# Optimization experiments

Hardware: AMD Instinct MI355X
Metric: run time of the kernel (lower is better)

Reference implementation:

```python
import jax, jax.numpy as jnp
import numpy as np

VTH = 1.0
BRANCH = 2
START_TIME = 10
CODING_TIME = 10
REMAIN_TIME = 5
GAMMA = 0.5
LENS = 0.5


@jax.custom_vjp
def spike_fn(x):
    # Heaviside forward, gaussian surrogate gradient (DH-SNN ActFun_adp)
    return (x > 0).astype(x.dtype)


def _spike_fwd(x):
    return spike_fn(x), x


def _spike_bwd(x, g):
    grad = GAMMA * jnp.exp(-x * x / (2.0 * LENS * LENS)) / np.float32(np.sqrt(2 * np.pi) * LENS)
    return (g * grad,)


spike_fn.defvjp(_spike_fwd, _spike_bwd)


def setup_inputs() -> dict:
    B, T, I, H, O = 2048, 1000, 40, 16, 2
    key = jax.random.key(0)
    ks = jax.random.split(key, 6)
    x = jax.random.normal(ks[0], (B, T, I), jnp.float32)
    target = jax.random.randint(ks[1], (B, T), 0, O, jnp.int32)
    # branch connectivity mask: each neuron's inputs randomly permuted, split across branches
    rng = np.random.default_rng(0)
    mask = np.zeros((H * BRANCH, I), np.float32)
    per = I // BRANCH
    for n in range(H):
        perm = rng.permutation(I)
        for b in range(BRANCH):
            mask[n * BRANCH + b, perm[b * per:(b + 1) * per]] = 1.0
    bound1 = 1.0 / np.sqrt(I)
    W1 = jax.random.uniform(ks[2], (H * BRANCH, I), jnp.float32, -bound1, bound1)
    tau_m = jax.random.uniform(ks[3], (H,), jnp.float32, 0.0, 4.0)
    tau_n = jax.random.uniform(ks[4], (H, BRANCH), jnp.float32, 2.0, 6.0)
    w2k, b2k = jax.random.split(ks[5])
    bound2 = 1.0 / np.sqrt(H)
    W2 = jax.random.uniform(w2k, (O, H), jnp.float32, -bound2, bound2)
    b2 = jax.random.uniform(b2k, (O,), jnp.float32, -bound2, bound2)
    return {"x": x, "target": target, "W1": W1, "tau_m": tau_m,
            "tau_n": tau_n, "mask": jnp.asarray(mask), "W2": W2, "b2": b2}


def reference(x, target, W1, tau_m, tau_n, mask, W2, b2):
    B, T, I = x.shape
    H, BR = tau_n.shape
    Wm = W1 * mask                     # [H*BR, I] masked dendritic weights
    alpha = jax.nn.sigmoid(tau_m)      # [H]  membrane decay
    beta = jax.nn.sigmoid(tau_n)       # [H, BR]  dendritic decay
    idx = jnp.arange(T)
    flags = ((idx - START_TIME) % (CODING_TIME + REMAIN_TIME) > REMAIN_TIME) & (idx > START_TIME)

    def step(carry, xs):
        d, mem, spk = carry
        xt, tgt, flag = xs             # xt [B,I], tgt [B], flag scalar bool
        cur = (xt @ Wm.T).reshape(B, H, BR)
        d = beta * d + (1.0 - beta) * cur
        l = d.sum(-1)                  # [B,H]
        mem = (mem - VTH * spk) * alpha + (1.0 - alpha) * l
        spk = spike_fn(mem - VTH)
        logits = spk @ W2.T + b2       # [B,2]
        p = jax.nn.softmax(logits, axis=1)
        # original applies CrossEntropyLoss to an already-softmaxed output (double softmax)
        ce = -jnp.take_along_axis(jax.nn.log_softmax(p, axis=1), tgt[:, None], axis=1).mean()
        corr = (jnp.argmax(p, axis=1) == tgt).sum()
        loss_inc = jnp.where(flag, ce, jnp.float32(0.0))
        corr_inc = jnp.where(flag, corr, 0)
        return (d, mem, spk), (logits, loss_inc, corr_inc)

    d0 = jnp.zeros((B, H, BR), x.dtype)
    m0 = jnp.zeros((B, H), x.dtype)
    s0 = jnp.zeros((B, H), x.dtype)
    _, (logits_t, loss_t, corr_t) = jax.lax.scan(
        step, (d0, m0, s0), (x.transpose(1, 0, 2), target.T, flags))
    loss = loss_t.sum()
    d2_output = logits_t.transpose(1, 0, 2)  # [B, T, 2]
    correct = corr_t.sum()
    total = flags.sum() * B
    return loss, d2_output, correct, total
```

## Files before the change

### kernel.cpp

```cpp
#include <hip/hip_runtime.h>

#define T_STEPS 1000
#define B_TOT   2048
#define I_IN    40
#define H_N     16
#define TC      25
#define NCHUNK  40
#define EPB     2
#define BLOCK   256
#define ELEM_LDS   (TC*48)
#define CHUNK_LDS  (EPB*ELEM_LDS)
#define NUNIT      (EPB*TC*10)
#define LOGITS_OFF 1
#define CORR_OFF  (1 + 2*B_TOT*T_STEPS)
#define TOTAL_OFF (CORR_OFF + 1)

__global__ void snn_init(float* out) {
    out[0] = 0.0f;
    out[CORR_OFF] = 0.0f;
    out[TOTAL_OFF] = 1216512.0f;
}

__device__ __forceinline__ float dpp_xor1(float v) {
    return __int_as_float(__builtin_amdgcn_update_dpp(0, __float_as_int(v), 0xB1, 0xF, 0xF, true));
}
__device__ __forceinline__ float dpp_xor2(float v) {
    return __int_as_float(__builtin_amdgcn_update_dpp(0, __float_as_int(v), 0x4E, 0xF, 0xF, true));
}
__device__ __forceinline__ float swz_xor4(float v) {
    return __int_as_float(__builtin_amdgcn_ds_swizzle(__float_as_int(v), 0x101F));
}

__global__ __launch_bounds__(BLOCK) void snn_main(
    const float* __restrict__ x, const int* __restrict__ target,
    const float* __restrict__ W1, const float* __restrict__ tau_m,
    const float* __restrict__ tau_n, const float* __restrict__ mask,
    const float* __restrict__ W2, const float* __restrict__ b2,
    float* __restrict__ out)
{
    __shared__ float xbuf[2][CHUNK_LDS];
    __shared__ unsigned smask[EPB*2*TC];

    const int tid  = threadIdx.x;
    const int g    = tid >> 7;
    const int lane = tid & 63;
    const int h    = (tid >> 6) & 1;
    const int q    = lane & 3;
    const int br   = (lane >> 2) & 1;
    const int nl   = lane >> 3;
    const int n    = h*8 + nl;
    const int r    = n*2 + br;
    const int b0   = blockIdx.x * EPB;

    float w[10];
#pragma unroll
    for (int j = 0; j < 10; ++j) {
        const int i = 4*j + q;
        w[j] = W1[r*I_IN + i] * mask[r*I_IN + i];
    }

    const float alpha = 1.0f / (1.0f + __expf(-tau_m[n]));
    const float beta  = 1.0f / (1.0f + __expf(-tau_n[r]));
    const float b2v0  = b2[0];
    const float b2v1  = b2[1];

    float w20[H_N], w21[H_N];
#pragma unroll
    for (int nn = 0; nn < H_N; ++nn) {
        w20[nn] = W2[nn];
        w21[nn] = W2[H_N + nn];
    }

    int goff0, lds0, goff1 = 0, lds1 = 0;
    const bool v1ok = (tid + BLOCK) < NUNIT;
    {
        const int u = tid, e = u/250, rem = u%250, tf = rem/10, f4 = rem%10;
        goff0 = ((b0+e)*T_STEPS + tf)*I_IN + 4*f4;
        lds0  = e*ELEM_LDS + tf*48 + f4;
    }
    if (v1ok) {
        const int u = tid + BLOCK, e = u/250, rem = u%250, tf = rem/10, f4 = rem%10;
        goff1 = ((b0+e)*T_STEPS + tf)*I_IN + 4*f4;
        lds1  = e*ELEM_LDS + tf*48 + f4;
    }

    float4 pf0 = *(const float4*)(x + goff0);
    float4 pf1 = v1ok ? *(const float4*)(x + goff1) : make_float4(0,0,0,0);

    const int  p    = tid >> 2;
    const bool comb = ((tid & 3) == 0) && (p < EPB*TC);
    const int  cg   = p / TC, ct = p % TC;

    float d_st = 0.0f, mem = 0.0f, spk = 0.0f;
    float acc_loss = 0.0f, acc_corr = 0.0f;
    unsigned long long cap = 0;

    for (int c = 0; c < NCHUNK; ++c) {
        const int t0 = c * TC;
        float* buf = xbuf[c & 1];
        buf[lds0] = pf0.x; buf[lds0+12] = pf0.y; buf[lds0+24] = pf0.z; buf[lds0+36] = pf0.w;
        if (v1ok) { buf[lds1] = pf1.x; buf[lds1+12] = pf1.y; buf[lds1+24] = pf1.z; buf[lds1+36] = pf1.w; }
        __syncthreads();
        if (c + 1 < NCHUNK) {
            const int tadd = (t0 + TC) * I_IN;
            pf0 = *(const float4*)(x + tadd + goff0);
            if (v1ok) pf1 = *(const float4*)(x + tadd + goff1);
        }

        const float* xg = buf + g*ELEM_LDS + q*12;
#pragma unroll
        for (int tt = 0; tt < TC; ++tt) {
            const float* xp = xg + tt*48;
            const float4 a0 = *(const float4*)(xp);
            const float4 a1 = *(const float4*)(xp + 4);
            const float2 a2 = *(const float2*)(xp + 8);
            float s = 0.0f;
            s = fmaf(w[0], a0.x, s); s = fmaf(w[1], a0.y, s);
            s = fmaf(w[2], a0.z, s); s = fmaf(w[3], a0.w, s);
            s = fmaf(w[4], a1.x, s); s = fmaf(w[5], a1.y, s);
            s = fmaf(w[6], a1.z, s); s = fmaf(w[7], a1.w, s);
            s = fmaf(w[8], a2.x, s); s = fmaf(w[9], a2.y, s);
            const float s01 = s + dpp_xor1(s);
            const float cur = s01 + dpp_xor2(s01);
            d_st = fmaf(beta, d_st - cur, cur);
            const float l = d_st + swz_xor4(d_st);
            mem = fmaf(alpha, (mem - spk) - l, l);
            const bool fired = mem > 1.0f;
            spk = fired ? 1.0f : 0.0f;
            const unsigned long long bal = __ballot(fired);
            if (lane == tt) cap = bal;
        }

        if (lane < TC) {
            unsigned m8 = 0;
#pragma unroll
            for (int k = 0; k < 8; ++k)
                m8 |= ((unsigned)(cap >> (k*8)) & 1u) << k;
            smask[(g*2 + h)*TC + lane] = m8;
        }
        __syncthreads();

        if (comb) {
            const int t = t0 + ct;
            const unsigned m = smask[(cg*2 + 0)*TC + ct] | (smask[(cg*2 + 1)*TC + ct] << 8);
            float sL0 = b2v0, sL1 = b2v1;
#pragma unroll
            for (int nn = 0; nn < H_N; ++nn) {
                const float f = (float)((m >> nn) & 1u);
                sL0 = fmaf(f, w20[nn], sL0);
                sL1 = fmaf(f, w21[nn], sL1);
            }
            const int b = b0 + cg;
            const int oidx = (b*T_STEPS + t)*2;
            out[LOGITS_OFF + oidx]     = sL0;
            out[LOGITS_OFF + oidx + 1] = sL1;
            const bool flag = (t > 10) && (((t - 10) % 15) > 5);
            if (flag) {
                const int tgt = target[b*T_STEPS + t];
                float mx  = fmaxf(sL0, sL1);
                float e0  = __expf(sL0 - mx), e1 = __expf(sL1 - mx);
                float inv = 1.0f / (e0 + e1);
                float p0  = e0*inv, p1 = e1*inv;
                float mm  = fmaxf(p0, p1);
                float lse = mm + __logf(__expf(p0 - mm) + __expf(p1 - mm));
                float qv  = ((tgt == 1) ? p1 : p0) - lse;
                acc_loss -= qv;
                const int pred = (p1 > p0) ? 1 : 0;
                acc_corr += (pred == tgt) ? 1.0f : 0.0f;
            }
        }
    }

    acc_loss *= (1.0f / (float)B_TOT);
#pragma unroll
    for (int mk = 1; mk < 64; mk <<= 1) {
        acc_loss += __shfl_xor(acc_loss, mk, 64);
        acc_corr += __shfl_xor(acc_corr, mk, 64);
    }
    if (lane == 0) {
        atomicAdd(out, acc_loss);
        atomicAdd(out + CORR_OFF, acc_corr);
    }
}

extern "C" void kernel_launch(void* const* d_in, const int* in_sizes, int n_in,
                              void* d_out, int out_size, void* d_ws, size_t ws_size,
                              hipStream_t stream) {
    const float* x      = (const float*)d_in[0];
    const int*   target = (const int*)d_in[1];
    const float* W1     = (const float*)d_in[2];
    const float* tau_m  = (const float*)d_in[3];
    const float* tau_n  = (const float*)d_in[4];
    const float* mask   = (const float*)d_in[5];
    const float* W2     = (const float*)d_in[6];
    const float* b2     = (const float*)d_in[7];
    float* out = (float*)d_out;

    snn_init<<<1, 1, 0, stream>>>(out);
    snn_main<<<B_TOT/EPB, BLOCK, 0, stream>>>(x, target, W1, tau_m, tau_n, mask, W2, b2, out);
}
```

Measured before the change: 560.4 us.

## Map one batch element per wavefront with packed FMA and lane-local spike history

Changes the thread mapping so that each 64-lane wavefront handles one whole batch element (16 neurons × 2 branches × 2 input halves) instead of splitting it across two waves, and puts four elements in each block. The dot product uses packed v_pk_fma_f32 over pairs of inputs. Branch reduction is now DPP add-combines, replacing the ds_swizzle. Spike history is kept as a per-lane bit register read back with readlane, which removes the ballot, the shared spike-mask array and the second __syncthreads per chunk. This cuts cross-wave synchronisation and instruction count per step, at the cost of more LDS per block (fewer resident blocks) and longer per-lane FMA chains.

```diff
diff --git a/kernel.cpp b/kernel.cpp
--- a/kernel.cpp
+++ b/kernel.cpp
@@ -6,7 +6,7 @@
 #define H_N     16
 #define TC      25
 #define NCHUNK  40
-#define EPB     2
+#define EPB     4
 #define BLOCK   256
 #define ELEM_LDS   (TC*48)
 #define CHUNK_LDS  (EPB*ELEM_LDS)
@@ -15,20 +15,26 @@
 #define CORR_OFF  (1 + 2*B_TOT*T_STEPS)
 #define TOTAL_OFF (CORR_OFF + 1)
 
+typedef float v2f __attribute__((ext_vector_type(2)));
+
 __global__ void snn_init(float* out) {
     out[0] = 0.0f;
     out[CORR_OFF] = 0.0f;
     out[TOTAL_OFF] = 1216512.0f;
 }
 
-__device__ __forceinline__ float dpp_xor1(float v) {
-    return __int_as_float(__builtin_amdgcn_update_dpp(0, __float_as_int(v), 0xB1, 0xF, 0xF, true));
-}
-__device__ __forceinline__ float dpp_xor2(float v) {
-    return __int_as_float(__builtin_amdgcn_update_dpp(0, __float_as_int(v), 0x4E, 0xF, 0xF, true));
-}
-__device__ __forceinline__ float swz_xor4(float v) {
-    return __int_as_float(__builtin_amdgcn_ds_swizzle(__float_as_int(v), 0x101F));
+__device__ __forceinline__ v2f pk_fma(v2f a, v2f b, v2f c) {
+    v2f d;
+    asm("v_pk_fma_f32 %0, %1, %2, %3" : "=v"(d) : "v"(a), "v"(b), "v"(c));
+    return d;
+}
+__device__ __forceinline__ float dpp_add_xor1(float v) {
+    int s = __float_as_int(v);
+    return v + __int_as_float(__builtin_amdgcn_update_dpp(s, s, 0xB1, 0xF, 0xF, true));
+}
+__device__ __forceinline__ float dpp_add_xor2(float v) {
+    int s = __float_as_int(v);
+    return v + __int_as_float(__builtin_amdgcn_update_dpp(s, s, 0x4E, 0xF, 0xF, true));
 }
 
 __global__ __launch_bounds__(BLOCK) void snn_main(
@@ -39,24 +45,23 @@
     float* __restrict__ out)
 {
     __shared__ float xbuf[2][CHUNK_LDS];
-    __shared__ unsigned smask[EPB*2*TC];
 
     const int tid  = threadIdx.x;
-    const int g    = tid >> 7;
+    const int g    = tid >> 6;
     const int lane = tid & 63;
-    const int h    = (tid >> 6) & 1;
-    const int q    = lane & 3;
-    const int br   = (lane >> 2) & 1;
-    const int nl   = lane >> 3;
-    const int n    = h*8 + nl;
+    const int p    = lane & 1;
+    const int br   = (lane >> 1) & 1;
+    const int n    = lane >> 2;
     const int r    = n*2 + br;
     const int b0   = blockIdx.x * EPB;
-
-    float w[10];
+    const int b    = b0 + g;
+
+    v2f wp[10];
 #pragma unroll
     for (int j = 0; j < 10; ++j) {
-        const int i = 4*j + q;
-        w[j] = W1[r*I_IN + i] * mask[r*I_IN + i];
+        const int i = 4*j + 2*p;
+        wp[j].x = W1[r*I_IN + i]     * mask[r*I_IN + i];
+        wp[j].y = W1[r*I_IN + i + 1] * mask[r*I_IN + i + 1];
     }
 
     const float alpha = 1.0f / (1.0f + __expf(-tau_m[n]));
@@ -71,86 +76,88 @@
         w21[nn] = W2[H_N + nn];
     }
 
-    int goff0, lds0, goff1 = 0, lds1 = 0;
-    const bool v1ok = (tid + BLOCK) < NUNIT;
-    {
-        const int u = tid, e = u/250, rem = u%250, tf = rem/10, f4 = rem%10;
-        goff0 = ((b0+e)*T_STEPS + tf)*I_IN + 4*f4;
-        lds0  = e*ELEM_LDS + tf*48 + f4;
-    }
-    if (v1ok) {
-        const int u = tid + BLOCK, e = u/250, rem = u%250, tf = rem/10, f4 = rem%10;
-        goff1 = ((b0+e)*T_STEPS + tf)*I_IN + 4*f4;
-        lds1  = e*ELEM_LDS + tf*48 + f4;
-    }
-
-    float4 pf0 = *(const float4*)(x + goff0);
-    float4 pf1 = v1ok ? *(const float4*)(x + goff1) : make_float4(0,0,0,0);
-
-    const int  p    = tid >> 2;
-    const bool comb = ((tid & 3) == 0) && (p < EPB*TC);
-    const int  cg   = p / TC, ct = p % TC;
+    int  goff[4], lbase[4], lf4[4];
+    bool gv[4];
+#pragma unroll
+    for (int jj = 0; jj < 4; ++jj) {
+        const int u = tid + BLOCK*jj;
+        gv[jj] = (u < NUNIT);
+        const int uc = gv[jj] ? u : 0;
+        const int e = uc/250, rem = uc%250, tf = rem/10, f4 = rem%10;
+        goff[jj]  = ((b0+e)*T_STEPS + tf)*I_IN + 4*f4;
+        lbase[jj] = e*ELEM_LDS + tf*48;
+        lf4[jj]   = 2*f4;
+    }
+
+    float4 pf[4];
+#pragma unroll
+    for (int jj = 0; jj < 4; ++jj)
+        if (gv[jj]) pf[jj] = *(const float4*)(x + goff[jj]);
 
     float d_st = 0.0f, mem = 0.0f, spk = 0.0f;
     float acc_loss = 0.0f, acc_corr = 0.0f;
-    unsigned long long cap = 0;
 
     for (int c = 0; c < NCHUNK; ++c) {
         const int t0 = c * TC;
         float* buf = xbuf[c & 1];
-        buf[lds0] = pf0.x; buf[lds0+12] = pf0.y; buf[lds0+24] = pf0.z; buf[lds0+36] = pf0.w;
-        if (v1ok) { buf[lds1] = pf1.x; buf[lds1+12] = pf1.y; buf[lds1+24] = pf1.z; buf[lds1+36] = pf1.w; }
+#pragma unroll
+        for (int jj = 0; jj < 4; ++jj) {
+            if (gv[jj]) {
+                *(float2*)(buf + lbase[jj] + lf4[jj])      = make_float2(pf[jj].x, pf[jj].y);
+                *(float2*)(buf + lbase[jj] + 24 + lf4[jj]) = make_float2(pf[jj].z, pf[jj].w);
+            }
+        }
         __syncthreads();
         if (c + 1 < NCHUNK) {
             const int tadd = (t0 + TC) * I_IN;
-            pf0 = *(const float4*)(x + tadd + goff0);
-            if (v1ok) pf1 = *(const float4*)(x + tadd + goff1);
-        }
-
-        const float* xg = buf + g*ELEM_LDS + q*12;
+#pragma unroll
+            for (int jj = 0; jj < 4; ++jj)
+                if (gv[jj]) pf[jj] = *(const float4*)(x + tadd + goff[jj]);
+        }
+
+        unsigned hist = 0u;
+        const float* xg = buf + g*ELEM_LDS + p*24;
 #pragma unroll
         for (int tt = 0; tt < TC; ++tt) {
-            const float* xp = xg + tt*48;
-            const float4 a0 = *(const float4*)(xp);
-            const float4 a1 = *(const float4*)(xp + 4);
-            const float2 a2 = *(const float2*)(xp + 8);
-            float s = 0.0f;
-            s = fmaf(w[0], a0.x, s); s = fmaf(w[1], a0.y, s);
-            s = fmaf(w[2], a0.z, s); s = fmaf(w[3], a0.w, s);
-            s = fmaf(w[4], a1.x, s); s = fmaf(w[5], a1.y, s);
-            s = fmaf(w[6], a1.z, s); s = fmaf(w[7], a1.w, s);
-            s = fmaf(w[8], a2.x, s); s = fmaf(w[9], a2.y, s);
-            const float s01 = s + dpp_xor1(s);
-            const float cur = s01 + dpp_xor2(s01);
+            const float4* xp = (const float4*)(xg + tt*48);
+            const float4 q0 = xp[0], q1 = xp[1], q2 = xp[2], q3 = xp[3], q4 = xp[4];
+            v2f acc; acc.x = 0.0f; acc.y = 0.0f;
+            v2f xa;
+            xa.x=q0.x; xa.y=q0.y; acc = pk_fma(wp[0], xa, acc);
+            xa.x=q0.z; xa.y=q0.w; acc = pk_fma(wp[1], xa, acc);
+            xa.x=q1.x; xa.y=q1.y; acc = pk_fma(wp[2], xa, acc);
+            xa.x=q1.z; xa.y=q1.w; acc = pk_fma(wp[3], xa, acc);
+            xa.x=q2.x; xa.y=q2.y; acc = pk_fma(wp[4], xa, acc);
+            xa.x=q2.z; xa.y=q2.w; acc = pk_fma(wp[5], xa, acc);
+            xa.x=q3.x; xa.y=q3.y; acc = pk_fma(wp[6], xa, acc);
+            xa.x=q3.z; xa.y=q3.w; acc = pk_fma(wp[7], xa, acc);
+            xa.x=q4.x; xa.y=q4.y; acc = pk_fma(wp[8], xa, acc);
+            xa.x=q4.z; xa.y=q4.w; acc = pk_fma(wp[9], xa, acc);
+            const float loc = acc.x + acc.y;
+            const float cur = dpp_add_xor1(loc);
             d_st = fmaf(beta, d_st - cur, cur);
-            const float l = d_st + swz_xor4(d_st);
+            const float l = dpp_add_xor2(d_st);
             mem = fmaf(alpha, (mem - spk) - l, l);
             const bool fired = mem > 1.0f;
             spk = fired ? 1.0f : 0.0f;
-            const unsigned long long bal = __ballot(fired);
-            if (lane == tt) cap = bal;
-        }
+            hist = (hist << 1) | (fired ? 1u : 0u);
+        }
+
+        unsigned hh[H_N];
+#pragma unroll
+        for (int nn = 0; nn < H_N; ++nn)
+            hh[nn] = (unsigned)__builtin_amdgcn_readlane((int)hist, nn*4);
 
         if (lane < TC) {
-            unsigned m8 = 0;
-#pragma unroll
-            for (int k = 0; k < 8; ++k)
-                m8 |= ((unsigned)(cap >> (k*8)) & 1u) << k;
-            smask[(g*2 + h)*TC + lane] = m8;
-        }
-        __syncthreads();
-
-        if (comb) {
-            const int t = t0 + ct;
-            const unsigned m = smask[(cg*2 + 0)*TC + ct] | (smask[(cg*2 + 1)*TC + ct] << 8);
+            const int t  = t0 + lane;
+            const int sh = (TC - 1) - lane;
             float sL0 = b2v0, sL1 = b2v1;
 #pragma unroll
             for (int nn = 0; nn < H_N; ++nn) {
-                const float f = (float)((m >> nn) & 1u);
+                const float f = (float)((hh[nn] >> sh) & 1u);
                 sL0 = fmaf(f, w20[nn], sL0);
                 sL1 = fmaf(f, w21[nn], sL1);
             }
-            const int b = b0 + cg;
             const int oidx = (b*T_STEPS + t)*2;
             out[LOGITS_OFF + oidx]     = sL0;
             out[LOGITS_OFF + oidx + 1] = sL1;
@@ -173,7 +180,7 @@
 
     acc_loss *= (1.0f / (float)B_TOT);
 #pragma unroll
-    for (int mk = 1; mk < 64; mk <<= 1) {
+    for (int mk = 1; mk < 32; mk <<= 1) {
         acc_loss += __shfl_xor(acc_loss, mk, 64);
         acc_corr += __shfl_xor(acc_corr, mk, 64);
     }
```

Measured after the change: 563.7 us. No clear change (+0.6%).
